# Performance work log

Hardware: AMD Instinct MI355X
Metric: run time of the kernel (lower is better)

Reference implementation:

```python
import jax, jax.numpy as jnp
import numpy as np

N, D = 8192, 256
TEMP = 0.07


def setup_inputs() -> dict:
    key = jax.random.key(0)
    kx, ky = jax.random.split(key)
    x = jax.random.normal(kx, (N, D), dtype=jnp.float32)
    y = jax.random.normal(ky, (N, D), dtype=jnp.float32)
    # L2-normalize (standard for InfoNCE; keeps exp(sim/temp) finite)
    x = x / jnp.linalg.norm(x, axis=-1, keepdims=True)
    y = y / jnp.linalg.norm(y, axis=-1, keepdims=True)
    return {"x": x, "y": y}


def reference(x, y):
    # sim_matrix = exp(x @ y^T / temperature), shape [N, N]
    sim = jnp.exp(jnp.matmul(x, y.T) / TEMP)
    # positives: exp(<x_i, y_i>/T) == diagonal of sim
    l_pos = jnp.exp(jnp.sum(x * y, axis=-1) / TEMP)
    # negatives: row-sum excluding the diagonal (equivalent to masked_select)
    l_neg = jnp.sum(sim, axis=-1) - jnp.diagonal(sim)
    loss = jnp.mean(-jnp.log(l_pos / l_neg))
    return loss
```

## Files before the change

### kernel.cpp

```cpp
#include <hip/hip_runtime.h>
#include <hip/hip_bf16.h>

#define N_ROWS 8192
#define D_DIM  256

static constexpr float kQuantScale = 64.0f;
static constexpr float kScaleAcc = 20.609929155556627f / 4096.0f;
static constexpr float kInvTAcc  = 14.285714285714286f / 4096.0f;

typedef float f32x4 __attribute__((ext_vector_type(4)));
typedef long  lx2   __attribute__((ext_vector_type(2)));

__device__ __forceinline__ void gl_lds16(const void* g, void* l) {
  __builtin_amdgcn_global_load_lds(
      (const __attribute__((address_space(1))) void*)g,
      (__attribute__((address_space(3))) void*)l, 16, 0, 0);
}

__global__ __launch_bounds__(256)
void cvt_fp8_kernel(const float* __restrict__ x, const float* __restrict__ y,
                    unsigned char* __restrict__ xq, unsigned char* __restrict__ yq,
                    float* __restrict__ rowsum, float* __restrict__ out) {
  if (blockIdx.x == 0) {
    for (int i = threadIdx.x; i < N_ROWS; i += 256) rowsum[i] = 0.f;
    if (threadIdx.x == 0) out[0] = 0.f;
  }
  const int per_mat = N_ROWS * D_DIM / 8;
  int idx = blockIdx.x * blockDim.x + threadIdx.x;
  const float* src = x;
  unsigned char* dst = xq;
  int i = idx;
  if (idx >= per_mat) { src = y; dst = yq; i = idx - per_mat; }
  float4 a = ((const float4*)src)[2 * (size_t)i];
  float4 b = ((const float4*)src)[2 * (size_t)i + 1];
  int v0 = 0, v1 = 0;
  v0 = __builtin_amdgcn_cvt_pk_fp8_f32(a.x * kQuantScale, a.y * kQuantScale, v0, false);
  v0 = __builtin_amdgcn_cvt_pk_fp8_f32(a.z * kQuantScale, a.w * kQuantScale, v0, true);
  v1 = __builtin_amdgcn_cvt_pk_fp8_f32(b.x * kQuantScale, b.y * kQuantScale, v1, false);
  v1 = __builtin_amdgcn_cvt_pk_fp8_f32(b.z * kQuantScale, b.w * kQuantScale, v1, true);
  const int row = i >> 5;
  const int c   = i & 31;
  const int s   = c >> 2, q = c & 3;
  const size_t off = (size_t)row * D_DIM + q * 64 + s * 8;
  *(int2*)(dst + off) = make_int2(v0, v1);
}

__global__ __launch_bounds__(256, 2)
void infonce_gemm(const unsigned char* __restrict__ X,
                  const unsigned char* __restrict__ Y,
                  float* __restrict__ rowsum, float* __restrict__ diag) {
  constexpr int BM = 128, BKB = 128;
  __shared__ unsigned char Xs[2][BM * BKB];
  __shared__ unsigned char Ys[2][BM * BKB];

  const int b  = blockIdx.x;
  const int bi = b >> 3;
  const int gj = b & 7;

  const int t    = threadIdx.x;
  const int lane = t & 63;
  const int wave = t >> 6;
  const int wm   = wave >> 1;
  const int wn   = wave & 1;
  const int quad = lane >> 4;
  const int l15  = lane & 15;

  const unsigned char* Xblk = X + (size_t)(bi * BM) * D_DIM;

  int srow[4], scg[4], sc0[4];
#pragma unroll
  for (int it = 0; it < 4; ++it) {
    const int c0 = (it * 4 + wave) * 64;
    const int s  = c0 + lane;
    sc0[it] = c0;
    srow[it] = s >> 3;
    scg[it]  = (s & 7) ^ ((s >> 3) & 7);
  }

  f32x4 acc[4][4];
#pragma unroll
  for (int a = 0; a < 4; ++a)
#pragma unroll
    for (int c = 0; c < 4; ++c) acc[a][c] = (f32x4){0.f, 0.f, 0.f, 0.f};

  {
    const unsigned char* Yblk = Y + (size_t)((gj * 8 + 0) * BM) * D_DIM;
#pragma unroll
    for (int it = 0; it < 4; ++it) {
      const size_t go = (size_t)srow[it] * D_DIM + ((scg[it] >> 1) << 6) + ((scg[it] & 1) << 4);
      gl_lds16(Xblk + go, &Xs[0][sc0[it] * 16]);
      gl_lds16(Yblk + go, &Ys[0][sc0[it] * 16]);
    }
  }

  for (int r = 0; r < 16; ++r) {
    const int tt = r >> 1;
    const int h  = r & 1;
    const int p  = r & 1;

    __syncthreads();

    if (r < 15) {
      const int nt_ = (r + 1) >> 1, nh = (r + 1) & 1, np = (r + 1) & 1;
      const unsigned char* Yblk = Y + (size_t)((gj * 8 + nt_) * BM) * D_DIM;
      const int hofs = nh * 32;
#pragma unroll
      for (int it = 0; it < 4; ++it) {
        const size_t go = (size_t)srow[it] * D_DIM + ((scg[it] >> 1) << 6) + hofs + ((scg[it] & 1) << 4);
        gl_lds16(Xblk + go, &Xs[np][sc0[it] * 16]);
        gl_lds16(Yblk + go, &Ys[np][sc0[it] * 16]);
      }
    }

#pragma unroll
    for (int u2 = 0; u2 < 2; ++u2) {
      lx2 af[4], bfr[4];
#pragma unroll
      for (int mt = 0; mt < 4; ++mt) {
        int row = wm * 64 + mt * 16 + l15;
        int chs = (quad * 2 + u2) ^ (row & 7);
        af[mt] = *(const lx2*)(&Xs[p][row * BKB + chs * 16]);
      }
#pragma unroll
      for (int nt = 0; nt < 4; ++nt) {
        int row = wn * 64 + nt * 16 + l15;
        int chs = (quad * 2 + u2) ^ (row & 7);
        bfr[nt] = *(const lx2*)(&Ys[p][row * BKB + chs * 16]);
      }
#pragma unroll
      for (int sub = 0; sub < 2; ++sub)
#pragma unroll
        for (int mt = 0; mt < 4; ++mt)
#pragma unroll
          for (int nt = 0; nt < 4; ++nt)
            acc[mt][nt] = __builtin_amdgcn_mfma_f32_16x16x32_fp8_fp8(
                af[mt][sub], bfr[nt][sub], acc[mt][nt], 0, 0, 0);
    }

    if (h == 1) {
      const int bj = gj * 8 + tt;
      const int gi_base = bi * BM + wm * 64;
#pragma unroll
      for (int mt = 0; mt < 4; ++mt) {
#pragma unroll
        for (int rr = 0; rr < 4; ++rr) {
          float part = 0.f;
#pragma unroll
          for (int nt = 0; nt < 4; ++nt)
            part += __builtin_amdgcn_exp2f(acc[mt][nt][rr] * kScaleAcc);
          part += __shfl_xor(part, 1);
          part += __shfl_xor(part, 2);
          part += __shfl_xor(part, 4);
          part += __shfl_xor(part, 8);
          if (l15 == 0) atomicAdd(&rowsum[gi_base + mt * 16 + quad * 4 + rr], part);
        }
      }
      if (bi == bj && wm == wn) {
#pragma unroll
        for (int mt = 0; mt < 4; ++mt) {
#pragma unroll
          for (int rr = 0; rr < 4; ++rr) {
            if (l15 == quad * 4 + rr)
              diag[gi_base + mt * 16 + l15] = acc[mt][mt][rr];
          }
        }
      }
#pragma unroll
      for (int a = 0; a < 4; ++a)
#pragma unroll
        for (int c = 0; c < 4; ++c) acc[a][c] = (f32x4){0.f, 0.f, 0.f, 0.f};
    }
  }
}

__global__ __launch_bounds__(128)
void finalize_kernel(const float* __restrict__ rowsum,
                     const float* __restrict__ diag, float* __restrict__ out) {
  const int i = blockIdx.x * 128 + threadIdx.x;
  const float d  = diag[i];
  const float ed = __builtin_amdgcn_exp2f(d * kScaleAcc);
  float v = __logf(rowsum[i] - ed) - d * kInvTAcc;
  v += __shfl_xor(v, 1);
  v += __shfl_xor(v, 2);
  v += __shfl_xor(v, 4);
  v += __shfl_xor(v, 8);
  v += __shfl_xor(v, 16);
  v += __shfl_xor(v, 32);
  if ((threadIdx.x & 63) == 0)
    atomicAdd(out, v * (1.0f / (float)N_ROWS));
}

extern "C" void kernel_launch(void* const* d_in, const int* in_sizes, int n_in,
                              void* d_out, int out_size, void* d_ws, size_t ws_size,
                              hipStream_t stream) {
  const float* x = (const float*)d_in[0];
  const float* y = (const float*)d_in[1];
  float* out = (float*)d_out;

  float* rowsum = (float*)d_ws;
  float* diag   = rowsum + N_ROWS;
  unsigned char* xq = (unsigned char*)d_ws + 2 * N_ROWS * sizeof(float) + 16;
  unsigned char* yq = xq + (size_t)N_ROWS * D_DIM;

  int cvt_blocks = 2 * N_ROWS * D_DIM / 8 / 256;
  cvt_fp8_kernel<<<cvt_blocks, 256, 0, stream>>>(x, y, xq, yq, rowsum, out);

  infonce_gemm<<<512, 256, 0, stream>>>(xq, yq, rowsum, diag);

  finalize_kernel<<<N_ROWS / 128, 128, 0, stream>>>(rowsum, diag, out);
}
```

Baseline: 120.7 us.

## Enlarge GEMM tile to 256x256 with 8 waves and K-slab pipelining

The fused exp-rowsum GEMM now uses 256-row tiles, 512-thread blocks (8 waves, each computing 128x64) and 64-byte K slabs over four stages per Y tile, instead of 128x128 tiles with 128-byte slabs. The fp8 conversion kernel writes a matching interleaved K layout, and the LDS swizzle is rebuilt for 64-byte rows. The goal is more data reuse per LDS load, fewer Y re-reads per X tile, and fewer row-sum atomics per element. The costs are higher register pressure from 32 accumulators per wave, more barriers because the K steps are shorter, and only 256 blocks, which may fill the CUs unevenly.

```diff
diff --git a/kernel.cpp b/kernel.cpp
--- a/kernel.cpp
+++ b/kernel.cpp
@@ -40,18 +40,20 @@
   v1 = __builtin_amdgcn_cvt_pk_fp8_f32(b.z * kQuantScale, b.w * kQuantScale, v1, true);
   const int row = i >> 5;
   const int c   = i & 31;
-  const int s   = c >> 2, q = c & 3;
-  const size_t off = (size_t)row * D_DIM + q * 64 + s * 8;
+  const int ug  = c >> 2;
+  const int q   = c & 3;
+  const int rh  = ug >> 1;
+  const int u   = ug & 1;
+  const size_t off = (size_t)row * D_DIM + rh * 64 + q * 16 + u * 8;
   *(int2*)(dst + off) = make_int2(v0, v1);
 }
 
-__global__ __launch_bounds__(256, 2)
+__global__ __launch_bounds__(512, 2)
 void infonce_gemm(const unsigned char* __restrict__ X,
                   const unsigned char* __restrict__ Y,
                   float* __restrict__ rowsum, float* __restrict__ diag) {
-  constexpr int BM = 128, BKB = 128;
-  __shared__ unsigned char Xs[2][BM * BKB];
-  __shared__ unsigned char Ys[2][BM * BKB];
+  __shared__ unsigned char Xs[2][256 * 64];
+  __shared__ unsigned char Ys[2][256 * 64];
 
   const int b  = blockIdx.x;
   const int bi = b >> 3;
@@ -60,88 +62,88 @@
   const int t    = threadIdx.x;
   const int lane = t & 63;
   const int wave = t >> 6;
-  const int wm   = wave >> 1;
-  const int wn   = wave & 1;
+  const int wm   = wave >> 2;
+  const int wn   = wave & 3;
   const int quad = lane >> 4;
   const int l15  = lane & 15;
 
-  const unsigned char* Xblk = X + (size_t)(bi * BM) * D_DIM;
-
-  int srow[4], scg[4], sc0[4];
-#pragma unroll
-  for (int it = 0; it < 4; ++it) {
-    const int c0 = (it * 4 + wave) * 64;
+  const unsigned char* Xblk = X + (size_t)(bi * 256) * D_DIM;
+
+  int sc0[2], srow[2], scg[2];
+#pragma unroll
+  for (int it = 0; it < 2; ++it) {
+    const int c0 = (it * 8 + wave) * 64;
     const int s  = c0 + lane;
-    sc0[it] = c0;
-    srow[it] = s >> 3;
-    scg[it]  = (s & 7) ^ ((s >> 3) & 7);
-  }
-
-  f32x4 acc[4][4];
-#pragma unroll
-  for (int a = 0; a < 4; ++a)
+    const int row = s >> 2;
+    sc0[it]  = c0;
+    srow[it] = row;
+    scg[it]  = (s & 3) ^ ((row >> 1) & 3);
+  }
+
+  f32x4 acc[8][4];
+#pragma unroll
+  for (int a = 0; a < 8; ++a)
 #pragma unroll
     for (int c = 0; c < 4; ++c) acc[a][c] = (f32x4){0.f, 0.f, 0.f, 0.f};
 
   {
-    const unsigned char* Yblk = Y + (size_t)((gj * 8 + 0) * BM) * D_DIM;
-#pragma unroll
-    for (int it = 0; it < 4; ++it) {
-      const size_t go = (size_t)srow[it] * D_DIM + ((scg[it] >> 1) << 6) + ((scg[it] & 1) << 4);
+    const unsigned char* Yblk = Y + (size_t)((gj * 4) * 256) * D_DIM;
+#pragma unroll
+    for (int it = 0; it < 2; ++it) {
+      const size_t go = (size_t)srow[it] * D_DIM + scg[it] * 16;
       gl_lds16(Xblk + go, &Xs[0][sc0[it] * 16]);
       gl_lds16(Yblk + go, &Ys[0][sc0[it] * 16]);
     }
   }
 
+#pragma unroll 4
   for (int r = 0; r < 16; ++r) {
-    const int tt = r >> 1;
-    const int h  = r & 1;
+    const int tt = r >> 2;
+    const int rh = r & 3;
     const int p  = r & 1;
 
     __syncthreads();
 
     if (r < 15) {
-      const int nt_ = (r + 1) >> 1, nh = (r + 1) & 1, np = (r + 1) & 1;
-      const unsigned char* Yblk = Y + (size_t)((gj * 8 + nt_) * BM) * D_DIM;
-      const int hofs = nh * 32;
-#pragma unroll
-      for (int it = 0; it < 4; ++it) {
-        const size_t go = (size_t)srow[it] * D_DIM + ((scg[it] >> 1) << 6) + hofs + ((scg[it] & 1) << 4);
-        gl_lds16(Xblk + go, &Xs[np][sc0[it] * 16]);
-        gl_lds16(Yblk + go, &Ys[np][sc0[it] * 16]);
+      const int rn = r + 1;
+      const int ttn = rn >> 2, rhn = rn & 3, pn = rn & 1;
+      const unsigned char* Yblk = Y + (size_t)((gj * 4 + ttn) * 256) * D_DIM;
+      const int kofs = rhn * 64;
+#pragma unroll
+      for (int it = 0; it < 2; ++it) {
+        const size_t go = (size_t)srow[it] * D_DIM + kofs + scg[it] * 16;
+        gl_lds16(Xblk + go, &Xs[pn][sc0[it] * 16]);
+        gl_lds16(Yblk + go, &Ys[pn][sc0[it] * 16]);
       }
     }
 
-#pragma unroll
-    for (int u2 = 0; u2 < 2; ++u2) {
-      lx2 af[4], bfr[4];
-#pragma unroll
-      for (int mt = 0; mt < 4; ++mt) {
-        int row = wm * 64 + mt * 16 + l15;
-        int chs = (quad * 2 + u2) ^ (row & 7);
-        af[mt] = *(const lx2*)(&Xs[p][row * BKB + chs * 16]);
-      }
-#pragma unroll
-      for (int nt = 0; nt < 4; ++nt) {
-        int row = wn * 64 + nt * 16 + l15;
-        int chs = (quad * 2 + u2) ^ (row & 7);
-        bfr[nt] = *(const lx2*)(&Ys[p][row * BKB + chs * 16]);
-      }
-#pragma unroll
-      for (int sub = 0; sub < 2; ++sub)
-#pragma unroll
-        for (int mt = 0; mt < 4; ++mt)
-#pragma unroll
-          for (int nt = 0; nt < 4; ++nt)
-            acc[mt][nt] = __builtin_amdgcn_mfma_f32_16x16x32_fp8_fp8(
-                af[mt][sub], bfr[nt][sub], acc[mt][nt], 0, 0, 0);
-    }
-
-    if (h == 1) {
-      const int bj = gj * 8 + tt;
-      const int gi_base = bi * BM + wm * 64;
-#pragma unroll
-      for (int mt = 0; mt < 4; ++mt) {
+    lx2 af[8], bfr[4];
+#pragma unroll
+    for (int mt = 0; mt < 8; ++mt) {
+      int row = wm * 128 + mt * 16 + l15;
+      int pp  = quad ^ ((row >> 1) & 3);
+      af[mt] = *(const lx2*)(&Xs[p][row * 64 + pp * 16]);
+    }
+#pragma unroll
+    for (int nt = 0; nt < 4; ++nt) {
+      int row = wn * 64 + nt * 16 + l15;
+      int pp  = quad ^ ((row >> 1) & 3);
+      bfr[nt] = *(const lx2*)(&Ys[p][row * 64 + pp * 16]);
+    }
+#pragma unroll
+    for (int sub = 0; sub < 2; ++sub)
+#pragma unroll
+      for (int mt = 0; mt < 8; ++mt)
+#pragma unroll
+        for (int nt = 0; nt < 4; ++nt)
+          acc[mt][nt] = __builtin_amdgcn_mfma_f32_16x16x32_fp8_fp8(
+              af[mt][sub], bfr[nt][sub], acc[mt][nt], 0, 0, 0);
+
+    if (rh == 3) {
+      const int bj = gj * 4 + tt;
+      const int gi_base = bi * 256 + wm * 128;
+#pragma unroll
+      for (int mt = 0; mt < 8; ++mt) {
 #pragma unroll
         for (int rr = 0; rr < 4; ++rr) {
           float part = 0.f;
@@ -155,18 +157,19 @@
           if (l15 == 0) atomicAdd(&rowsum[gi_base + mt * 16 + quad * 4 + rr], part);
         }
       }
-      if (bi == bj && wm == wn) {
-#pragma unroll
-        for (int mt = 0; mt < 4; ++mt) {
+      if (bi == bj && (wn >> 1) == wm) {
+#pragma unroll
+        for (int nt = 0; nt < 4; ++nt) {
+          const int mtd = (wn & 1) * 4 + nt;
 #pragma unroll
           for (int rr = 0; rr < 4; ++rr) {
             if (l15 == quad * 4 + rr)
-              diag[gi_base + mt * 16 + l15] = acc[mt][mt][rr];
+              diag[gi_base + mtd * 16 + l15] = acc[mtd][nt][rr];
           }
         }
       }
 #pragma unroll
-      for (int a = 0; a < 4; ++a)
+      for (int a = 0; a < 8; ++a)
 #pragma unroll
         for (int c = 0; c < 4; ++c) acc[a][c] = (f32x4){0.f, 0.f, 0.f, 0.f};
     }
@@ -205,7 +208,7 @@
   int cvt_blocks = 2 * N_ROWS * D_DIM / 8 / 256;
   cvt_fp8_kernel<<<cvt_blocks, 256, 0, stream>>>(x, y, xq, yq, rowsum, out);
 
-  infonce_gemm<<<512, 256, 0, stream>>>(xq, yq, rowsum, diag);
+  infonce_gemm<<<256, 512, 0, stream>>>(xq, yq, rowsum, diag);
 
   finalize_kernel<<<N_ROWS / 128, 128, 0, stream>>>(rowsum, diag, out);
 }
```

New measurement: 298.6 us. +147.3%, slower.

## Use 256-row X tiles resident in LDS and fuse finalize via last-block ticket

Applied to the files above, without the earlier changes.

The GEMM now runs 256 blocks of 512 threads. Each block keeps a full 256x256 FP8 X tile resident in LDS and streams double-buffered full-K 128-row Y tiles, so X no longer has to be reloaded for every K half. The conversion kernel's output layout and the swizzle change to match the full-K LDS layout. The separate finalize kernel is removed: the last block to finish, found through an atomic ticket counter, computes the loss reduction, saving a launch at the cost of a serial tail and lower occupancy (one block per CU with about 128KB of LDS).

```diff
diff --git a/kernel.cpp b/kernel.cpp
--- a/kernel.cpp
+++ b/kernel.cpp
@@ -20,10 +20,10 @@
 __global__ __launch_bounds__(256)
 void cvt_fp8_kernel(const float* __restrict__ x, const float* __restrict__ y,
                     unsigned char* __restrict__ xq, unsigned char* __restrict__ yq,
-                    float* __restrict__ rowsum, float* __restrict__ out) {
+                    float* __restrict__ rowsum, unsigned int* __restrict__ done) {
   if (blockIdx.x == 0) {
     for (int i = threadIdx.x; i < N_ROWS; i += 256) rowsum[i] = 0.f;
-    if (threadIdx.x == 0) out[0] = 0.f;
+    if (threadIdx.x == 0) *done = 0u;
   }
   const int per_mat = N_ROWS * D_DIM / 8;
   int idx = blockIdx.x * blockDim.x + threadIdx.x;
@@ -40,18 +40,20 @@
   v1 = __builtin_amdgcn_cvt_pk_fp8_f32(b.z * kQuantScale, b.w * kQuantScale, v1, true);
   const int row = i >> 5;
   const int c   = i & 31;
-  const int s   = c >> 2, q = c & 3;
-  const size_t off = (size_t)row * D_DIM + q * 64 + s * 8;
+  const int ks  = c >> 2;
+  const int q   = c & 3;
+  const size_t off = (size_t)row * D_DIM + (ks >> 1) * 64 + q * 16 + (ks & 1) * 8;
   *(int2*)(dst + off) = make_int2(v0, v1);
 }
 
-__global__ __launch_bounds__(256, 2)
+__global__ __launch_bounds__(512, 1)
 void infonce_gemm(const unsigned char* __restrict__ X,
                   const unsigned char* __restrict__ Y,
-                  float* __restrict__ rowsum, float* __restrict__ diag) {
-  constexpr int BM = 128, BKB = 128;
-  __shared__ unsigned char Xs[2][BM * BKB];
-  __shared__ unsigned char Ys[2][BM * BKB];
+                  float* __restrict__ rowsum, float* __restrict__ diag,
+                  unsigned int* __restrict__ done, float* __restrict__ out) {
+  __shared__ unsigned char Xs[256 * 256];
+  __shared__ unsigned char Ys[2][128 * 256];
+  __shared__ unsigned int ticket_s;
 
   const int b  = blockIdx.x;
   const int bi = b >> 3;
@@ -65,16 +67,26 @@
   const int quad = lane >> 4;
   const int l15  = lane & 15;
 
-  const unsigned char* Xblk = X + (size_t)(bi * BM) * D_DIM;
-
-  int srow[4], scg[4], sc0[4];
-#pragma unroll
-  for (int it = 0; it < 4; ++it) {
-    const int c0 = (it * 4 + wave) * 64;
-    const int s  = c0 + lane;
-    sc0[it] = c0;
-    srow[it] = s >> 3;
-    scg[it]  = (s & 7) ^ ((s >> 3) & 7);
+  const unsigned char* Xblk = X + (size_t)(bi * 256) * D_DIM;
+
+#pragma unroll
+  for (int it = 0; it < 8; ++it) {
+    const int c0  = (it * 8 + wave) * 64;
+    const int s   = c0 + lane;
+    const int row = s >> 4;
+    const int cg  = (s & 15) ^ (row & 15);
+    gl_lds16(Xblk + (size_t)row * D_DIM + cg * 16, &Xs[c0 * 16]);
+  }
+  {
+    const unsigned char* Yblk = Y + (size_t)(gj * 8) * 128 * D_DIM;
+#pragma unroll
+    for (int it = 0; it < 4; ++it) {
+      const int c0  = (it * 8 + wave) * 64;
+      const int s   = c0 + lane;
+      const int row = s >> 4;
+      const int cg  = (s & 15) ^ (row & 15);
+      gl_lds16(Yblk + (size_t)row * D_DIM + cg * 16, &Ys[0][c0 * 16]);
+    }
   }
 
   f32x4 acc[4][4];
@@ -83,49 +95,37 @@
 #pragma unroll
     for (int c = 0; c < 4; ++c) acc[a][c] = (f32x4){0.f, 0.f, 0.f, 0.f};
 
-  {
-    const unsigned char* Yblk = Y + (size_t)((gj * 8 + 0) * BM) * D_DIM;
-#pragma unroll
-    for (int it = 0; it < 4; ++it) {
-      const size_t go = (size_t)srow[it] * D_DIM + ((scg[it] >> 1) << 6) + ((scg[it] & 1) << 4);
-      gl_lds16(Xblk + go, &Xs[0][sc0[it] * 16]);
-      gl_lds16(Yblk + go, &Ys[0][sc0[it] * 16]);
-    }
-  }
-
-  for (int r = 0; r < 16; ++r) {
-    const int tt = r >> 1;
-    const int h  = r & 1;
-    const int p  = r & 1;
+  for (int tt = 0; tt < 8; ++tt) {
+    const int p = tt & 1;
 
     __syncthreads();
 
-    if (r < 15) {
-      const int nt_ = (r + 1) >> 1, nh = (r + 1) & 1, np = (r + 1) & 1;
-      const unsigned char* Yblk = Y + (size_t)((gj * 8 + nt_) * BM) * D_DIM;
-      const int hofs = nh * 32;
+    if (tt < 7) {
+      const unsigned char* Yblk = Y + (size_t)(gj * 8 + tt + 1) * 128 * D_DIM;
 #pragma unroll
       for (int it = 0; it < 4; ++it) {
-        const size_t go = (size_t)srow[it] * D_DIM + ((scg[it] >> 1) << 6) + hofs + ((scg[it] & 1) << 4);
-        gl_lds16(Xblk + go, &Xs[np][sc0[it] * 16]);
-        gl_lds16(Yblk + go, &Ys[np][sc0[it] * 16]);
-      }
-    }
-
-#pragma unroll
-    for (int u2 = 0; u2 < 2; ++u2) {
+        const int c0  = (it * 8 + wave) * 64;
+        const int s   = c0 + lane;
+        const int row = s >> 4;
+        const int cg  = (s & 15) ^ (row & 15);
+        gl_lds16(Yblk + (size_t)row * D_DIM + cg * 16, &Ys[p ^ 1][c0 * 16]);
+      }
+    }
+
+#pragma unroll
+    for (int g = 0; g < 4; ++g) {
       lx2 af[4], bfr[4];
 #pragma unroll
       for (int mt = 0; mt < 4; ++mt) {
-        int row = wm * 64 + mt * 16 + l15;
-        int chs = (quad * 2 + u2) ^ (row & 7);
-        af[mt] = *(const lx2*)(&Xs[p][row * BKB + chs * 16]);
+        const int row = wm * 64 + mt * 16 + l15;
+        const int pos = (g * 4 + quad) ^ l15;
+        af[mt] = *(const lx2*)(&Xs[row * 256 + pos * 16]);
       }
 #pragma unroll
       for (int nt = 0; nt < 4; ++nt) {
-        int row = wn * 64 + nt * 16 + l15;
-        int chs = (quad * 2 + u2) ^ (row & 7);
-        bfr[nt] = *(const lx2*)(&Ys[p][row * BKB + chs * 16]);
+        const int row = wn * 64 + nt * 16 + l15;
+        const int pos = (g * 4 + quad) ^ l15;
+        bfr[nt] = *(const lx2*)(&Ys[p][row * 256 + pos * 16]);
       }
 #pragma unroll
       for (int sub = 0; sub < 2; ++sub)
@@ -137,57 +137,61 @@
                 af[mt][sub], bfr[nt][sub], acc[mt][nt], 0, 0, 0);
     }
 
-    if (h == 1) {
-      const int bj = gj * 8 + tt;
-      const int gi_base = bi * BM + wm * 64;
-#pragma unroll
-      for (int mt = 0; mt < 4; ++mt) {
-#pragma unroll
-        for (int rr = 0; rr < 4; ++rr) {
-          float part = 0.f;
-#pragma unroll
-          for (int nt = 0; nt < 4; ++nt)
-            part += __builtin_amdgcn_exp2f(acc[mt][nt][rr] * kScaleAcc);
-          part += __shfl_xor(part, 1);
-          part += __shfl_xor(part, 2);
-          part += __shfl_xor(part, 4);
-          part += __shfl_xor(part, 8);
-          if (l15 == 0) atomicAdd(&rowsum[gi_base + mt * 16 + quad * 4 + rr], part);
-        }
-      }
-      if (bi == bj && wm == wn) {
-#pragma unroll
-        for (int mt = 0; mt < 4; ++mt) {
-#pragma unroll
-          for (int rr = 0; rr < 4; ++rr) {
+    const int gi_base = bi * 256 + wm * 64;
+#pragma unroll
+    for (int mt = 0; mt < 4; ++mt) {
+#pragma unroll
+      for (int rr = 0; rr < 4; ++rr) {
+        float part = 0.f;
+#pragma unroll
+        for (int nt = 0; nt < 4; ++nt)
+          part += __builtin_amdgcn_exp2f(acc[mt][nt][rr] * kScaleAcc);
+        part += __shfl_xor(part, 1);
+        part += __shfl_xor(part, 2);
+        part += __shfl_xor(part, 4);
+        part += __shfl_xor(part, 8);
+        if (l15 == 0) atomicAdd(&rowsum[gi_base + mt * 16 + quad * 4 + rr], part);
+      }
+    }
+    {
+      const int ct = gj * 8 + tt;
+      const bool d0 = (ct == 2 * bi)     && (wm == wn);
+      const bool d1 = (ct == 2 * bi + 1) && (wm == wn + 2);
+      if (d0 || d1) {
+#pragma unroll
+        for (int nt = 0; nt < 4; ++nt)
+#pragma unroll
+          for (int rr = 0; rr < 4; ++rr)
             if (l15 == quad * 4 + rr)
-              diag[gi_base + mt * 16 + l15] = acc[mt][mt][rr];
-          }
-        }
-      }
-#pragma unroll
-      for (int a = 0; a < 4; ++a)
-#pragma unroll
-        for (int c = 0; c < 4; ++c) acc[a][c] = (f32x4){0.f, 0.f, 0.f, 0.f};
-    }
-  }
-}
-
-__global__ __launch_bounds__(128)
-void finalize_kernel(const float* __restrict__ rowsum,
-                     const float* __restrict__ diag, float* __restrict__ out) {
-  const int i = blockIdx.x * 128 + threadIdx.x;
-  const float d  = diag[i];
-  const float ed = __builtin_amdgcn_exp2f(d * kScaleAcc);
-  float v = __logf(rowsum[i] - ed) - d * kInvTAcc;
-  v += __shfl_xor(v, 1);
-  v += __shfl_xor(v, 2);
-  v += __shfl_xor(v, 4);
-  v += __shfl_xor(v, 8);
-  v += __shfl_xor(v, 16);
-  v += __shfl_xor(v, 32);
-  if ((threadIdx.x & 63) == 0)
-    atomicAdd(out, v * (1.0f / (float)N_ROWS));
+              atomicExch(&diag[gi_base + nt * 16 + l15], acc[nt][nt][rr]);
+      }
+    }
+#pragma unroll
+    for (int a = 0; a < 4; ++a)
+#pragma unroll
+      for (int c = 0; c < 4; ++c) acc[a][c] = (f32x4){0.f, 0.f, 0.f, 0.f};
+  }
+
+  __syncthreads();
+  if (t == 0) ticket_s = atomicAdd(done, 1u);
+  __syncthreads();
+  if (ticket_s == 255u) {
+    __threadfence();
+    float local = 0.f;
+    for (int i = t; i < N_ROWS; i += 512) {
+      const float rs = atomicAdd(&rowsum[i], 0.0f);
+      const float d  = atomicAdd(&diag[i], 0.0f);
+      local += __logf(rs - __builtin_amdgcn_exp2f(d * kScaleAcc)) - d * kInvTAcc;
+    }
+    float* red = (float*)Xs;
+    red[t] = local;
+    __syncthreads();
+    for (int s2 = 256; s2 > 0; s2 >>= 1) {
+      if (t < s2) red[t] += red[t + s2];
+      __syncthreads();
+    }
+    if (t == 0) out[0] = red[0] / (float)N_ROWS;
+  }
 }
 
 extern "C" void kernel_launch(void* const* d_in, const int* in_sizes, int n_in,
@@ -199,13 +203,12 @@
 
   float* rowsum = (float*)d_ws;
   float* diag   = rowsum + N_ROWS;
+  unsigned int* done = (unsigned int*)(diag + N_ROWS);
   unsigned char* xq = (unsigned char*)d_ws + 2 * N_ROWS * sizeof(float) + 16;
   unsigned char* yq = xq + (size_t)N_ROWS * D_DIM;
 
   int cvt_blocks = 2 * N_ROWS * D_DIM / 8 / 256;
-  cvt_fp8_kernel<<<cvt_blocks, 256, 0, stream>>>(x, y, xq, yq, rowsum, out);
-
-  infonce_gemm<<<512, 256, 0, stream>>>(xq, yq, rowsum, diag);
-
-  finalize_kernel<<<N_ROWS / 128, 128, 0, stream>>>(rowsum, diag, out);
-}
+  cvt_fp8_kernel<<<cvt_blocks, 256, 0, stream>>>(x, y, xq, yq, rowsum, done);
+
+  infonce_gemm<<<256, 512, 0, stream>>>(xq, yq, rowsum, diag, done, out);
+}
```

After: 118.8 us. No clear change (-1.6%).
